# Optimization experiments

Measured on AMD Instinct MI355X. Metric: run time of the kernel, lower is better.

The kernel has to match this reference:

```python
import jax, jax.numpy as jnp
import numpy as np

N = 50000
IN_C, HID_C, OUT_C = 128, 64, 32
E = 800000
NEG_SLOPE = 0.2


def setup_inputs() -> dict:
    key = jax.random.key(0)
    ks = jax.random.split(key, 8)
    x = jax.random.normal(ks[0], (N, IN_C), dtype=jnp.float32)
    edge_index = jax.random.randint(ks[1], (2, E), 0, N, dtype=jnp.int64)
    # GATConv params (heads=1): lin weight, att_src/att_dst vectors, bias
    sc = 1.0 / np.sqrt(IN_C)
    W = jax.random.uniform(ks[2], (IN_C, HID_C), jnp.float32, -sc, sc)
    att_src = jax.random.normal(ks[3], (HID_C,), jnp.float32) * (1.0 / np.sqrt(HID_C))
    att_dst = jax.random.normal(ks[4], (HID_C,), jnp.float32) * (1.0 / np.sqrt(HID_C))
    bias_conv = jnp.zeros((HID_C,), jnp.float32)
    sl = 1.0 / np.sqrt(HID_C)
    W_lin = jax.random.uniform(ks[5], (HID_C, OUT_C), jnp.float32, -sl, sl)
    b_lin = jax.random.uniform(ks[6], (OUT_C,), jnp.float32, -sl, sl)
    return {"x": x, "edge_index": edge_index, "W": W, "att_src": att_src,
            "att_dst": att_dst, "bias_conv": bias_conv, "W_lin": W_lin, "b_lin": b_lin}


def reference(x, edge_index, W, att_src, att_dst, bias_conv, W_lin, b_lin):
    n = x.shape[0]
    h = x @ W  # [N, HID]
    # add self-loops (PyG GATConv default add_self_loops=True)
    loop = jnp.arange(n, dtype=edge_index.dtype)
    src = jnp.concatenate([edge_index[0], loop])  # [E+N]
    dst = jnp.concatenate([edge_index[1], loop])
    a_src = h @ att_src  # [N]
    a_dst = h @ att_dst
    e = jax.nn.leaky_relu(a_src[src] + a_dst[dst], NEG_SLOPE)  # [E+N]
    # segment softmax over incoming edges per destination node
    m = jax.ops.segment_max(e, dst, num_segments=n)
    e = jnp.exp(e - m[dst])
    denom = jax.ops.segment_sum(e, dst, num_segments=n)
    alpha = e / (denom[dst] + 1e-16)
    msg = alpha[:, None] * h[src]  # [E+N, HID]
    out = jax.ops.segment_sum(msg, dst, num_segments=n) + bias_conv
    out = jax.nn.relu(out)
    return out @ W_lin + b_lin
```

## Files before the change

### kernel.cpp

```cpp
#include <hip/hip_runtime.h>
#include <hip/hip_bf16.h>

#define IN_C  128
#define HID_C 64
#define OUT_C 32
#define NEG_SLOPE 0.2f
#define EPB1    2048
#define EPB2    2048
#define BUCKETW 64
#define RCAP    1536
#define SUPW    1024
#define RCAP1   18432
#define PARTS   9
#define CSTRIDE 16
#define XS_LD   136

typedef short bf16x8 __attribute__((ext_vector_type(8)));
typedef float f32x4  __attribute__((ext_vector_type(4)));

__device__ __forceinline__ unsigned short f2bf(float f) {
    __hip_bfloat16 h = __float2bfloat16(f);
    return *(unsigned short*)&h;
}
__device__ __forceinline__ float bflo(unsigned int u) {
    return __uint_as_float(u << 16);
}
__device__ __forceinline__ float bfhi(unsigned int u) {
    return __uint_as_float(u & 0xffff0000u);
}

__global__ __launch_bounds__(256) void gemm_mfma_kernel(
    const float* __restrict__ x, const float* __restrict__ W,
    const float* __restrict__ att_src, const float* __restrict__ att_dst,
    __hip_bfloat16* __restrict__ hb,
    float* __restrict__ a_src, float* __restrict__ a_dst,
    int* __restrict__ bcursor, int ncur, int n_nodes)
{
    __shared__ unsigned short xs[16 * XS_LD];
    __shared__ float redA[4][16];
    __shared__ float redD[4][16];
    const int t    = threadIdx.x;
    const int wv   = t >> 6;
    const int lane = t & 63;
    const int m16  = lane & 15;
    const int quad = lane >> 4;
    const int node0 = blockIdx.x * 16;
    const int nrows = min(16, n_nodes - node0);

    const int gid = blockIdx.x * 256 + t;
    if (gid < ncur) bcursor[gid] = 0;

    const int ncol = wv * 16 + m16;
    bf16x8 B[4];
#pragma unroll
    for (int k0 = 0; k0 < 4; ++k0)
#pragma unroll
        for (int j = 0; j < 8; ++j)
            B[k0][j] = (short)f2bf(W[(k0 * 32 + quad * 8 + j) * HID_C + ncol]);

    {
        const float4* xg = (const float4*)(x + (long)node0 * IN_C);
#pragma unroll
        for (int i = t; i < 512; i += 256) {
            const int row = i >> 5;
            const int c4  = i & 31;
            float4 v = (row < nrows) ? xg[i] : make_float4(0.f, 0.f, 0.f, 0.f);
            ushort4 u;
            u.x = f2bf(v.x); u.y = f2bf(v.y);
            u.z = f2bf(v.z); u.w = f2bf(v.w);
            *(ushort4*)(xs + row * XS_LD + c4 * 4) = u;
        }
    }
    __syncthreads();

    f32x4 C = {0.f, 0.f, 0.f, 0.f};
#pragma unroll
    for (int k0 = 0; k0 < 4; ++k0) {
        const bf16x8 A = *(const bf16x8*)(xs + m16 * XS_LD + k0 * 32 + quad * 8);
        C = __builtin_amdgcn_mfma_f32_16x16x32_bf16(A, B[k0], C, 0, 0, 0);
    }

#pragma unroll
    for (int r = 0; r < 4; ++r) {
        const int row = quad * 4 + r;
        if (row < nrows)
            hb[(long)(node0 + row) * HID_C + ncol] = __float2bfloat16(C[r]);
    }

    {
        const float av = att_src[ncol];
        const float dv = att_dst[ncol];
        float ps[4], pd[4];
#pragma unroll
        for (int r = 0; r < 4; ++r) { ps[r] = C[r] * av; pd[r] = C[r] * dv; }
#pragma unroll
        for (int off = 1; off <= 8; off <<= 1) {
#pragma unroll
            for (int r = 0; r < 4; ++r) {
                ps[r] += __shfl_xor(ps[r], off, 64);
                pd[r] += __shfl_xor(pd[r], off, 64);
            }
        }
        if (m16 == 0) {
#pragma unroll
            for (int r = 0; r < 4; ++r) {
                redA[wv][quad * 4 + r] = ps[r];
                redD[wv][quad * 4 + r] = pd[r];
            }
        }
    }
    __syncthreads();
    if (t < 16 && t < nrows) {
        a_src[node0 + t] = redA[0][t] + redA[1][t] + redA[2][t] + redA[3][t];
        a_dst[node0 + t] = redD[0][t] + redD[1][t] + redD[2][t] + redD[3][t];
    }
}

__global__ __launch_bounds__(256) void bin1_kernel(
    const int* __restrict__ ei, int E,
    int* __restrict__ bcur1, unsigned* __restrict__ superbuf)
{
    __shared__ unsigned stage[EPB1];
    __shared__ int excl[64];
    __shared__ int cur[64];
    __shared__ int gpos[64];

    const int t = threadIdx.x;
    const int base = blockIdx.x * EPB1;
    const int nedge = min(EPB1, E - base);

    if (t < 64) excl[t] = 0;
    __syncthreads();

    for (int i = t; i < nedge; i += 256)
        atomicAdd(&excl[ei[E + base + i] >> 10], 1);
    __syncthreads();

    if (t < 64) {
        int c = excl[t], incl = c;
#pragma unroll
        for (int off = 1; off <= 32; off <<= 1) {
            int u = __shfl_up(incl, off, 64);
            if (t >= off) incl += u;
        }
        excl[t] = incl - c;
        cur[t]  = incl - c;
    }
    __syncthreads();

    for (int i = t; i < nedge; i += 256) {
        const int s = ei[base + i];
        const int d = ei[E + base + i];
        const int sq = d >> 10;
        const int pos = atomicAdd(&cur[sq], 1);
        stage[pos] = (unsigned)s | ((unsigned)(d & 1023) << 16)
                     | ((unsigned)sq << 26);
    }
    __syncthreads();

    if (t < 64) {
        const int c = cur[t] - excl[t];
        gpos[t] = (c > 0) ? atomicAdd(&bcur1[t * CSTRIDE], c) : 0;
    }
    __syncthreads();

    for (int i = t; i < nedge; i += 256) {
        const unsigned r = stage[i];
        const int sq = r >> 26;
        const int dp = gpos[sq] + (i - excl[sq]);
        if (dp < RCAP1) superbuf[(long)sq * RCAP1 + dp] = r;
    }
}

__global__ __launch_bounds__(256) void bin2_kernel(
    const unsigned* __restrict__ superbuf, const int* __restrict__ bcur1,
    int* __restrict__ bcur2, unsigned* __restrict__ bucketbuf)
{
    __shared__ unsigned srt[EPB2];
    __shared__ int cnt[16];
    __shared__ int rp[16];
    __shared__ int cur16[16];
    __shared__ int gpos[16];

    const int t    = threadIdx.x;
    const int sq   = blockIdx.x / PARTS;
    const int part = blockIdx.x % PARTS;
    const int tot  = min(bcur1[sq * CSTRIDE], RCAP1);
    const int beg  = part * EPB2;
    const int n    = min(EPB2, tot - beg);
    if (n <= 0) return;

    if (t < 16) cnt[t] = 0;
    __syncthreads();

    const unsigned* src = superbuf + (long)sq * RCAP1 + beg;

    for (int i = t; i < n; i += 256)
        atomicAdd(&cnt[(src[i] >> 22) & 15], 1);
    __syncthreads();

    if (t == 0) {
        int run = 0;
#pragma unroll
        for (int k = 0; k < 16; ++k) { rp[k] = run; cur16[k] = run; run += cnt[k]; }
    }
    __syncthreads();

    for (int i = t; i < n; i += 256) {
        const unsigned r = src[i];
        const int pos = atomicAdd(&cur16[(r >> 22) & 15], 1);
        srt[pos] = r;
    }
    __syncthreads();

    if (t < 16) {
        const int c = cnt[t];
        const int q2 = sq * 16 + t;
        gpos[t] = (c > 0) ? atomicAdd(&bcur2[q2 * CSTRIDE], c) : 0;
    }
    __syncthreads();

    for (int i = t; i < n; i += 256) {
        const unsigned r = srt[i];
        const int idx = (r >> 22) & 15;
        const int dp  = gpos[idx] + (i - rp[idx]);
        const int q2  = sq * 16 + idx;
        const unsigned nx = (r & 0xFFFFu) | (((r >> 16) & 63u) << 16);
        if (dp < RCAP) bucketbuf[(long)q2 * RCAP + dp] = nx;
    }
}

__global__ __launch_bounds__(512) void bucket_agg_kernel(
    const unsigned* __restrict__ bucketbuf, const int* __restrict__ bcursor,
    const __hip_bfloat16* __restrict__ hb,
    const float* __restrict__ a_src, const float* __restrict__ a_dst,
    const float* __restrict__ bias_conv,
    const float* __restrict__ W_lin, const float* __restrict__ b_lin,
    float* __restrict__ out, int n_nodes)
{
    __shared__ unsigned srtL[RCAP];
    __shared__ int cntd[BUCKETW];
    __shared__ int rp[BUCKETW + 1];
    __shared__ int curd[BUCKETW];

    const int t  = threadIdx.x;
    const int q  = blockIdx.x;
    const int d0 = q * BUCKETW;
    const int dmax = min(BUCKETW, n_nodes - d0);
    const int tot  = min(bcursor[q * CSTRIDE], RCAP);
    const int wv = t >> 6, lane = t & 63, g8 = lane >> 3, l = lane & 7;

    if (t < BUCKETW) cntd[t] = 0;
    __syncthreads();

    const unsigned* gsrc = bucketbuf + (long)q * RCAP;

    for (int i = t; i < tot; i += 512)
        atomicAdd(&cntd[(gsrc[i] >> 16) & 63], 1);
    __syncthreads();

    if (t < 64) {
        int c = cntd[t], incl = c;
#pragma unroll
        for (int off = 1; off <= 32; off <<= 1) {
            int u = __shfl_up(incl, off, 64);
            if (t >= off) incl += u;
        }
        rp[t] = incl - c;
        curd[t] = incl - c;
        if (t == 63) rp[64] = incl;
    }
    __syncthreads();

    for (int i = t; i < tot; i += 512) {
        const unsigned r = gsrc[i];
        const int pos = atomicAdd(&curd[(r >> 16) & 63], 1);
        srtL[pos] = r;
    }
    __syncthreads();

    float Wr[8][4];
#pragma unroll
    for (int kc = 0; kc < 8; ++kc)
#pragma unroll
        for (int kj = 0; kj < 4; ++kj)
            Wr[kc][kj] = W_lin[(l * 8 + kc) * OUT_C + g8 * 4 + kj];
    float biasR[8];
#pragma unroll
    for (int kc = 0; kc < 8; ++kc) biasR[kc] = bias_conv[l * 8 + kc];
    float blinR[4];
#pragma unroll
    for (int kj = 0; kj < 4; ++kj) blinR[kj] = b_lin[g8 * 4 + kj];

    const unsigned short* hbs = (const unsigned short*)hb;

    for (int dloc = wv; dloc < dmax; dloc += 8) {
        const int d = d0 + dloc;
        const float ad = a_dst[d];
        float A[8] = {0.f,0.f,0.f,0.f,0.f,0.f,0.f,0.f};
        float den = 0.f;
        if (g8 == 0) {
            float e = a_src[d] + ad;
            e = (e >= 0.f) ? e : NEG_SLOPE * e;
            const float ws = __expf(e);
            const uint4 hv = *(const uint4*)(hbs + (long)d * HID_C + l * 8);
            den = ws;
            A[0] = ws * bflo(hv.x); A[1] = ws * bfhi(hv.x);
            A[2] = ws * bflo(hv.y); A[3] = ws * bfhi(hv.y);
            A[4] = ws * bflo(hv.z); A[5] = ws * bfhi(hv.z);
            A[6] = ws * bflo(hv.w); A[7] = ws * bfhi(hv.w);
        }
        const int beg = rp[dloc], fin = rp[dloc + 1];
        for (int j = beg + g8; j < fin; j += 16) {
            const int  j1   = j + 8;
            const bool has1 = j1 < fin;
            const unsigned r0 = srtL[j];
            const unsigned r1 = srtL[has1 ? j1 : j];
            const int   s0 = r0 & 0xFFFF;
            const int   s1 = r1 & 0xFFFF;
            const float as0 = a_src[s0];
            const float as1 = a_src[s1];
            const uint4 h0 = *(const uint4*)(hbs + (long)s0 * HID_C + l * 8);
            const uint4 h1 = *(const uint4*)(hbs + (long)s1 * HID_C + l * 8);
            float e0 = as0 + ad; e0 = (e0 >= 0.f) ? e0 : NEG_SLOPE * e0;
            float e1 = as1 + ad; e1 = (e1 >= 0.f) ? e1 : NEG_SLOPE * e1;
            const float w0 = __expf(e0);
            const float w1 = has1 ? __expf(e1) : 0.f;
            den += w0 + w1;
            A[0] = fmaf(w0, bflo(h0.x), A[0]); A[1] = fmaf(w0, bfhi(h0.x), A[1]);
            A[2] = fmaf(w0, bflo(h0.y), A[2]); A[3] = fmaf(w0, bfhi(h0.y), A[3]);
            A[4] = fmaf(w0, bflo(h0.z), A[4]); A[5] = fmaf(w0, bfhi(h0.z), A[5]);
            A[6] = fmaf(w0, bflo(h0.w), A[6]); A[7] = fmaf(w0, bfhi(h0.w), A[7]);
            A[0] = fmaf(w1, bflo(h1.x), A[0]); A[1] = fmaf(w1, bfhi(h1.x), A[1]);
            A[2] = fmaf(w1, bflo(h1.y), A[2]); A[3] = fmaf(w1, bfhi(h1.y), A[3]);
            A[4] = fmaf(w1, bflo(h1.z), A[4]); A[5] = fmaf(w1, bfhi(h1.z), A[5]);
            A[6] = fmaf(w1, bflo(h1.w), A[6]); A[7] = fmaf(w1, bfhi(h1.w), A[7]);
        }
#pragma unroll
        for (int off = 8; off <= 32; off <<= 1) {
#pragma unroll
            for (int k = 0; k < 8; ++k) A[k] += __shfl_xor(A[k], off, 64);
            den += __shfl_xor(den, off, 64);
        }
        const float rd = 1.0f / (den + 1e-16f);
        float p0 = 0.f, p1 = 0.f, p2 = 0.f, p3 = 0.f;
#pragma unroll
        for (int kc = 0; kc < 8; ++kc) {
            float vv = fmaf(A[kc], rd, biasR[kc]);
            vv = vv > 0.f ? vv : 0.f;
            p0 = fmaf(vv, Wr[kc][0], p0);
            p1 = fmaf(vv, Wr[kc][1], p1);
            p2 = fmaf(vv, Wr[kc][2], p2);
            p3 = fmaf(vv, Wr[kc][3], p3);
        }
#pragma unroll
        for (int off = 1; off <= 4; off <<= 1) {
            p0 += __shfl_xor(p0, off, 64);
            p1 += __shfl_xor(p1, off, 64);
            p2 += __shfl_xor(p2, off, 64);
            p3 += __shfl_xor(p3, off, 64);
        }
        if (l == 0) {
            float4 o = make_float4(p0 + blinR[0], p1 + blinR[1],
                                   p2 + blinR[2], p3 + blinR[3]);
            *(float4*)(out + (long)d * OUT_C + g8 * 4) = o;
        }
    }
}

extern "C" void kernel_launch(void* const* d_in, const int* in_sizes, int n_in,
                              void* d_out, int out_size, void* d_ws, size_t ws_size,
                              hipStream_t stream) {
    const float* x         = (const float*)d_in[0];
    const int*   ei        = (const int*)d_in[1];
    const float* W         = (const float*)d_in[2];
    const float* att_src   = (const float*)d_in[3];
    const float* att_dst   = (const float*)d_in[4];
    const float* bias_conv = (const float*)d_in[5];
    const float* W_lin     = (const float*)d_in[6];
    const float* b_lin     = (const float*)d_in[7];
    float*       out       = (float*)d_out;

    const int n_nodes = in_sizes[0] / IN_C;
    const int E       = in_sizes[1] / 2;
    const int B1   = (E + EPB1 - 1) / EPB1;
    const int Q    = (n_nodes + BUCKETW - 1) / BUCKETW;
    const int NSUP = (n_nodes + SUPW - 1) / SUPW;

    __hip_bfloat16* hb = (__hip_bfloat16*)d_ws;
    float* a_src   = (float*)(hb + (long)n_nodes * HID_C);
    float* a_dst   = a_src + n_nodes;
    int*   bcur1   = (int*)(a_dst + n_nodes);
    int*   bcur2   = bcur1 + NSUP * CSTRIDE;
    unsigned* superbuf  = (unsigned*)(bcur2 + (long)Q * CSTRIDE);
    unsigned* bucketbuf = superbuf + (long)NSUP * RCAP1;

    const int ncur = (NSUP + Q) * CSTRIDE;

    gemm_mfma_kernel<<<(n_nodes + 15) / 16, 256, 0, stream>>>(
        x, W, att_src, att_dst, hb, a_src, a_dst,
        bcur1, ncur, n_nodes);

    bin1_kernel<<<B1, 256, 0, stream>>>(ei, E, bcur1, superbuf);

    bin2_kernel<<<NSUP * PARTS, 256, 0, stream>>>(
        superbuf, bcur1, bcur2, bucketbuf);

    bucket_agg_kernel<<<Q, 512, 0, stream>>>(
        bucketbuf, bcur2, hb, a_src, a_dst,
        bias_conv, W_lin, b_lin, out, n_nodes);
}
```

Baseline: 158.6 us.

## Merge GEMM with first binning pass and drop second binning kernel

The node projection GEMM and the first edge-binning pass now run as one launch, with blocks split by index between the two roles, and the cursor zeroing moves to a memset. The second binning kernel is removed; each aggregation block instead scans its whole 1024-node super-bucket and filters the edges that belong to its 64-node bucket. This cuts one launch and one full write and read of the edge list, but each aggregation block now reads about 16 times more edge records, about 16K instead of about 1K.

Measured after the change: 177.8 us. 1.12x slower.

```diff
diff --git a/kernel.cpp b/kernel.cpp
--- a/kernel.cpp
+++ b/kernel.cpp
@@ -6,12 +6,10 @@
 #define OUT_C 32
 #define NEG_SLOPE 0.2f
 #define EPB1    2048
-#define EPB2    2048
 #define BUCKETW 64
 #define RCAP    1536
 #define SUPW    1024
 #define RCAP1   18432
-#define PARTS   9
 #define CSTRIDE 16
 #define XS_LD   136
 
@@ -29,209 +27,148 @@
     return __uint_as_float(u & 0xffff0000u);
 }
 
-__global__ __launch_bounds__(256) void gemm_mfma_kernel(
+__global__ __launch_bounds__(256) void gemm_bin1_kernel(
     const float* __restrict__ x, const float* __restrict__ W,
     const float* __restrict__ att_src, const float* __restrict__ att_dst,
     __hip_bfloat16* __restrict__ hb,
     float* __restrict__ a_src, float* __restrict__ a_dst,
-    int* __restrict__ bcursor, int ncur, int n_nodes)
+    const int* __restrict__ ei, int E,
+    int* __restrict__ bcur1, unsigned* __restrict__ superbuf,
+    int ngemm, int n_nodes)
 {
-    __shared__ unsigned short xs[16 * XS_LD];
-    __shared__ float redA[4][16];
-    __shared__ float redD[4][16];
-    const int t    = threadIdx.x;
-    const int wv   = t >> 6;
-    const int lane = t & 63;
-    const int m16  = lane & 15;
-    const int quad = lane >> 4;
-    const int node0 = blockIdx.x * 16;
-    const int nrows = min(16, n_nodes - node0);
-
-    const int gid = blockIdx.x * 256 + t;
-    if (gid < ncur) bcursor[gid] = 0;
-
-    const int ncol = wv * 16 + m16;
-    bf16x8 B[4];
-#pragma unroll
-    for (int k0 = 0; k0 < 4; ++k0)
-#pragma unroll
-        for (int j = 0; j < 8; ++j)
-            B[k0][j] = (short)f2bf(W[(k0 * 32 + quad * 8 + j) * HID_C + ncol]);
-
-    {
-        const float4* xg = (const float4*)(x + (long)node0 * IN_C);
-#pragma unroll
-        for (int i = t; i < 512; i += 256) {
-            const int row = i >> 5;
-            const int c4  = i & 31;
-            float4 v = (row < nrows) ? xg[i] : make_float4(0.f, 0.f, 0.f, 0.f);
-            ushort4 u;
-            u.x = f2bf(v.x); u.y = f2bf(v.y);
-            u.z = f2bf(v.z); u.w = f2bf(v.w);
-            *(ushort4*)(xs + row * XS_LD + c4 * 4) = u;
-        }
-    }
-    __syncthreads();
-
-    f32x4 C = {0.f, 0.f, 0.f, 0.f};
-#pragma unroll
-    for (int k0 = 0; k0 < 4; ++k0) {
-        const bf16x8 A = *(const bf16x8*)(xs + m16 * XS_LD + k0 * 32 + quad * 8);
-        C = __builtin_amdgcn_mfma_f32_16x16x32_bf16(A, B[k0], C, 0, 0, 0);
-    }
-
-#pragma unroll
-    for (int r = 0; r < 4; ++r) {
-        const int row = quad * 4 + r;
-        if (row < nrows)
-            hb[(long)(node0 + row) * HID_C + ncol] = __float2bfloat16(C[r]);
-    }
-
-    {
-        const float av = att_src[ncol];
-        const float dv = att_dst[ncol];
-        float ps[4], pd[4];
-#pragma unroll
-        for (int r = 0; r < 4; ++r) { ps[r] = C[r] * av; pd[r] = C[r] * dv; }
-#pragma unroll
-        for (int off = 1; off <= 8; off <<= 1) {
-#pragma unroll
-            for (int r = 0; r < 4; ++r) {
-                ps[r] += __shfl_xor(ps[r], off, 64);
-                pd[r] += __shfl_xor(pd[r], off, 64);
+    __shared__ __align__(16) unsigned char smem[8960];
+    const int t = threadIdx.x;
+
+    if ((int)blockIdx.x < ngemm) {
+        unsigned short* xs = (unsigned short*)smem;
+        float (*redA)[16] = (float(*)[16])(smem + 4352);
+        float (*redD)[16] = (float(*)[16])(smem + 4608);
+        const int wv   = t >> 6;
+        const int lane = t & 63;
+        const int m16  = lane & 15;
+        const int quad = lane >> 4;
+        const int node0 = blockIdx.x * 16;
+        const int nrows = min(16, n_nodes - node0);
+
+        const int ncol = wv * 16 + m16;
+        bf16x8 B[4];
+#pragma unroll
+        for (int k0 = 0; k0 < 4; ++k0)
+#pragma unroll
+            for (int j = 0; j < 8; ++j)
+                B[k0][j] = (short)f2bf(W[(k0 * 32 + quad * 8 + j) * HID_C + ncol]);
+
+        {
+            const float4* xg = (const float4*)(x + (long)node0 * IN_C);
+#pragma unroll
+            for (int i = t; i < 512; i += 256) {
+                const int row = i >> 5;
+                const int c4  = i & 31;
+                float4 v = (row < nrows) ? xg[i] : make_float4(0.f, 0.f, 0.f, 0.f);
+                ushort4 u;
+                u.x = f2bf(v.x); u.y = f2bf(v.y);
+                u.z = f2bf(v.z); u.w = f2bf(v.w);
+                *(ushort4*)(xs + row * XS_LD + c4 * 4) = u;
             }
         }
-        if (m16 == 0) {
-#pragma unroll
-            for (int r = 0; r < 4; ++r) {
-                redA[wv][quad * 4 + r] = ps[r];
-                redD[wv][quad * 4 + r] = pd[r];
+        __syncthreads();
+
+        f32x4 C = {0.f, 0.f, 0.f, 0.f};
+#pragma unroll
+        for (int k0 = 0; k0 < 4; ++k0) {
+            const bf16x8 A = *(const bf16x8*)(xs + m16 * XS_LD + k0 * 32 + quad * 8);
+            C = __builtin_amdgcn_mfma_f32_16x16x32_bf16(A, B[k0], C, 0, 0, 0);
+        }
+
+#pragma unroll
+        for (int r = 0; r < 4; ++r) {
+            const int row = quad * 4 + r;
+            if (row < nrows)
+                hb[(long)(node0 + row) * HID_C + ncol] = __float2bfloat16(C[r]);
+        }
+
+        {
+            const float av = att_src[ncol];
+            const float dv = att_dst[ncol];
+            float ps[4], pd[4];
+#pragma unroll
+            for (int r = 0; r < 4; ++r) { ps[r] = C[r] * av; pd[r] = C[r] * dv; }
+#pragma unroll
+            for (int off = 1; off <= 8; off <<= 1) {
+#pragma unroll
+                for (int r = 0; r < 4; ++r) {
+                    ps[r] += __shfl_xor(ps[r], off, 64);
+                    pd[r] += __shfl_xor(pd[r], off, 64);
+                }
             }
-        }
-    }
-    __syncthreads();
-    if (t < 16 && t < nrows) {
-        a_src[node0 + t] = redA[0][t] + redA[1][t] + redA[2][t] + redA[3][t];
-        a_dst[node0 + t] = redD[0][t] + redD[1][t] + redD[2][t] + redD[3][t];
-    }
-}
-
-__global__ __launch_bounds__(256) void bin1_kernel(
-    const int* __restrict__ ei, int E,
-    int* __restrict__ bcur1, unsigned* __restrict__ superbuf)
-{
-    __shared__ unsigned stage[EPB1];
-    __shared__ int excl[64];
-    __shared__ int cur[64];
-    __shared__ int gpos[64];
-
-    const int t = threadIdx.x;
-    const int base = blockIdx.x * EPB1;
-    const int nedge = min(EPB1, E - base);
-
-    if (t < 64) excl[t] = 0;
-    __syncthreads();
-
-    for (int i = t; i < nedge; i += 256)
-        atomicAdd(&excl[ei[E + base + i] >> 10], 1);
-    __syncthreads();
-
-    if (t < 64) {
-        int c = excl[t], incl = c;
-#pragma unroll
-        for (int off = 1; off <= 32; off <<= 1) {
-            int u = __shfl_up(incl, off, 64);
-            if (t >= off) incl += u;
-        }
-        excl[t] = incl - c;
-        cur[t]  = incl - c;
-    }
-    __syncthreads();
-
-    for (int i = t; i < nedge; i += 256) {
-        const int s = ei[base + i];
-        const int d = ei[E + base + i];
-        const int sq = d >> 10;
-        const int pos = atomicAdd(&cur[sq], 1);
-        stage[pos] = (unsigned)s | ((unsigned)(d & 1023) << 16)
-                     | ((unsigned)sq << 26);
-    }
-    __syncthreads();
-
-    if (t < 64) {
-        const int c = cur[t] - excl[t];
-        gpos[t] = (c > 0) ? atomicAdd(&bcur1[t * CSTRIDE], c) : 0;
-    }
-    __syncthreads();
-
-    for (int i = t; i < nedge; i += 256) {
-        const unsigned r = stage[i];
-        const int sq = r >> 26;
-        const int dp = gpos[sq] + (i - excl[sq]);
-        if (dp < RCAP1) superbuf[(long)sq * RCAP1 + dp] = r;
-    }
-}
-
-__global__ __launch_bounds__(256) void bin2_kernel(
+            if (m16 == 0) {
+#pragma unroll
+                for (int r = 0; r < 4; ++r) {
+                    redA[wv][quad * 4 + r] = ps[r];
+                    redD[wv][quad * 4 + r] = pd[r];
+                }
+            }
+        }
+        __syncthreads();
+        if (t < 16 && t < nrows) {
+            a_src[node0 + t] = redA[0][t] + redA[1][t] + redA[2][t] + redA[3][t];
+            a_dst[node0 + t] = redD[0][t] + redD[1][t] + redD[2][t] + redD[3][t];
+        }
+    } else {
+        unsigned* stage = (unsigned*)smem;
+        int* excl = (int*)(smem + 8192);
+        int* cur  = (int*)(smem + 8448);
+        int* gpos = (int*)(smem + 8704);
+
+        const int base = (blockIdx.x - ngemm) * EPB1;
+        const int nedge = min(EPB1, E - base);
+
+        if (t < 64) excl[t] = 0;
+        __syncthreads();
+
+        for (int i = t; i < nedge; i += 256)
+            atomicAdd(&excl[ei[E + base + i] >> 10], 1);
+        __syncthreads();
+
+        if (t < 64) {
+            int c = excl[t], incl = c;
+#pragma unroll
+            for (int off = 1; off <= 32; off <<= 1) {
+                int u = __shfl_up(incl, off, 64);
+                if (t >= off) incl += u;
+            }
+            excl[t] = incl - c;
+            cur[t]  = incl - c;
+        }
+        __syncthreads();
+
+        for (int i = t; i < nedge; i += 256) {
+            const int s = ei[base + i];
+            const int d = ei[E + base + i];
+            const int sq = d >> 10;
+            const int pos = atomicAdd(&cur[sq], 1);
+            stage[pos] = (unsigned)s | ((unsigned)(d & 1023) << 16)
+                         | ((unsigned)sq << 26);
+        }
+        __syncthreads();
+
+        if (t < 64) {
+            const int c = cur[t] - excl[t];
+            gpos[t] = (c > 0) ? atomicAdd(&bcur1[t * CSTRIDE], c) : 0;
+        }
+        __syncthreads();
+
+        for (int i = t; i < nedge; i += 256) {
+            const unsigned r = stage[i];
+            const int sq = r >> 26;
+            const int dp = gpos[sq] + (i - excl[sq]);
+            if (dp < RCAP1) superbuf[(long)sq * RCAP1 + dp] = r;
+        }
+    }
+}
+
+__global__ __launch_bounds__(512) void bucket_agg_kernel(
     const unsigned* __restrict__ superbuf, const int* __restrict__ bcur1,
-    int* __restrict__ bcur2, unsigned* __restrict__ bucketbuf)
-{
-    __shared__ unsigned srt[EPB2];
-    __shared__ int cnt[16];
-    __shared__ int rp[16];
-    __shared__ int cur16[16];
-    __shared__ int gpos[16];
-
-    const int t    = threadIdx.x;
-    const int sq   = blockIdx.x / PARTS;
-    const int part = blockIdx.x % PARTS;
-    const int tot  = min(bcur1[sq * CSTRIDE], RCAP1);
-    const int beg  = part * EPB2;
-    const int n    = min(EPB2, tot - beg);
-    if (n <= 0) return;
-
-    if (t < 16) cnt[t] = 0;
-    __syncthreads();
-
-    const unsigned* src = superbuf + (long)sq * RCAP1 + beg;
-
-    for (int i = t; i < n; i += 256)
-        atomicAdd(&cnt[(src[i] >> 22) & 15], 1);
-    __syncthreads();
-
-    if (t == 0) {
-        int run = 0;
-#pragma unroll
-        for (int k = 0; k < 16; ++k) { rp[k] = run; cur16[k] = run; run += cnt[k]; }
-    }
-    __syncthreads();
-
-    for (int i = t; i < n; i += 256) {
-        const unsigned r = src[i];
-        const int pos = atomicAdd(&cur16[(r >> 22) & 15], 1);
-        srt[pos] = r;
-    }
-    __syncthreads();
-
-    if (t < 16) {
-        const int c = cnt[t];
-        const int q2 = sq * 16 + t;
-        gpos[t] = (c > 0) ? atomicAdd(&bcur2[q2 * CSTRIDE], c) : 0;
-    }
-    __syncthreads();
-
-    for (int i = t; i < n; i += 256) {
-        const unsigned r = srt[i];
-        const int idx = (r >> 22) & 15;
-        const int dp  = gpos[idx] + (i - rp[idx]);
-        const int q2  = sq * 16 + idx;
-        const unsigned nx = (r & 0xFFFFu) | (((r >> 16) & 63u) << 16);
-        if (dp < RCAP) bucketbuf[(long)q2 * RCAP + dp] = nx;
-    }
-}
-
-__global__ __launch_bounds__(512) void bucket_agg_kernel(
-    const unsigned* __restrict__ bucketbuf, const int* __restrict__ bcursor,
     const __hip_bfloat16* __restrict__ hb,
     const float* __restrict__ a_src, const float* __restrict__ a_dst,
     const float* __restrict__ bias_conv,
@@ -243,20 +180,25 @@
     __shared__ int rp[BUCKETW + 1];
     __shared__ int curd[BUCKETW];
 
-    const int t  = threadIdx.x;
-    const int q  = blockIdx.x;
-    const int d0 = q * BUCKETW;
+    const int t   = threadIdx.x;
+    const int q   = blockIdx.x;
+    const int sq  = q >> 4;
+    const int idx = q & 15;
+    const int d0  = q * BUCKETW;
     const int dmax = min(BUCKETW, n_nodes - d0);
-    const int tot  = min(bcursor[q * CSTRIDE], RCAP);
+    const int tot  = min(bcur1[sq * CSTRIDE], RCAP1);
     const int wv = t >> 6, lane = t & 63, g8 = lane >> 3, l = lane & 7;
 
     if (t < BUCKETW) cntd[t] = 0;
     __syncthreads();
 
-    const unsigned* gsrc = bucketbuf + (long)q * RCAP;
-
-    for (int i = t; i < tot; i += 512)
-        atomicAdd(&cntd[(gsrc[i] >> 16) & 63], 1);
+    const unsigned* src = superbuf + (long)sq * RCAP1;
+
+    for (int i = t; i < tot; i += 512) {
+        const unsigned r = src[i];
+        if (((r >> 22) & 15) == (unsigned)idx)
+            atomicAdd(&cntd[(r >> 16) & 63], 1);
+    }
     __syncthreads();
 
     if (t < 64) {
@@ -273,9 +215,11 @@
     __syncthreads();
 
     for (int i = t; i < tot; i += 512) {
-        const unsigned r = gsrc[i];
-        const int pos = atomicAdd(&curd[(r >> 16) & 63], 1);
-        srtL[pos] = r;
+        const unsigned r = src[i];
+        if (((r >> 22) & 15) == (unsigned)idx) {
+            const int pos = atomicAdd(&curd[(r >> 16) & 63], 1);
+            if (pos < RCAP) srtL[pos] = r;
+        }
     }
     __syncthreads();
 
@@ -310,7 +254,8 @@
             A[4] = ws * bflo(hv.z); A[5] = ws * bfhi(hv.z);
             A[6] = ws * bflo(hv.w); A[7] = ws * bfhi(hv.w);
         }
-        const int beg = rp[dloc], fin = rp[dloc + 1];
+        const int beg = min(rp[dloc], RCAP);
+        const int fin = min(rp[dloc + 1], RCAP);
         for (int j = beg + g8; j < fin; j += 16) {
             const int  j1   = j + 8;
             const bool has1 = j1 < fin;
@@ -386,27 +331,21 @@
     const int B1   = (E + EPB1 - 1) / EPB1;
     const int Q    = (n_nodes + BUCKETW - 1) / BUCKETW;
     const int NSUP = (n_nodes + SUPW - 1) / SUPW;
+    const int NG   = (n_nodes + 15) / 16;
 
     __hip_bfloat16* hb = (__hip_bfloat16*)d_ws;
     float* a_src   = (float*)(hb + (long)n_nodes * HID_C);
     float* a_dst   = a_src + n_nodes;
     int*   bcur1   = (int*)(a_dst + n_nodes);
-    int*   bcur2   = bcur1 + NSUP * CSTRIDE;
-    unsigned* superbuf  = (unsigned*)(bcur2 + (long)Q * CSTRIDE);
-    unsigned* bucketbuf = superbuf + (long)NSUP * RCAP1;
-
-    const int ncur = (NSUP + Q) * CSTRIDE;
-
-    gemm_mfma_kernel<<<(n_nodes + 15) / 16, 256, 0, stream>>>(
+    unsigned* superbuf = (unsigned*)(bcur1 + NSUP * CSTRIDE);
+
+    hipMemsetAsync(bcur1, 0, (size_t)NSUP * CSTRIDE * sizeof(int), stream);
+
+    gemm_bin1_kernel<<<NG + B1, 256, 0, stream>>>(
         x, W, att_src, att_dst, hb, a_src, a_dst,
-        bcur1, ncur, n_nodes);
-
-    bin1_kernel<<<B1, 256, 0, stream>>>(ei, E, bcur1, superbuf);
-
-    bin2_kernel<<<NSUP * PARTS, 256, 0, stream>>>(
-        superbuf, bcur1, bcur2, bucketbuf);
+        ei, E, bcur1, superbuf, NG, n_nodes);
 
     bucket_agg_kernel<<<Q, 512, 0, stream>>>(
-        bucketbuf, bcur2, hb, a_src, a_dst,
+        superbuf, bcur1, hb, a_src, a_dst,
         bias_conv, W_lin, b_lin, out, n_nodes);
 }
```

## Fuse GEMM and first edge-binning pass into one heterogeneous kernel launch

Applied to the files above, without the earlier changes.

Merges the node-feature GEMM kernel and the first binning kernel into a single launch, with block ranges selecting which role each block plays and a shared byte buffer reinterpreted per role. The two stages are independent, so binning can overlap with the GEMM instead of waiting behind it, and one launch gap is removed. Cursor zeroing moves out of the GEMM into a separate memset, which adds a small extra operation on the stream.

New measurement: 156.0 us, median of 2. No clear change (-1.7%).

```diff
diff --git a/kernel.cpp b/kernel.cpp
--- a/kernel.cpp
+++ b/kernel.cpp
@@ -29,146 +29,143 @@
     return __uint_as_float(u & 0xffff0000u);
 }
 
-__global__ __launch_bounds__(256) void gemm_mfma_kernel(
+__global__ __launch_bounds__(256) void gemm_bin1_kernel(
     const float* __restrict__ x, const float* __restrict__ W,
     const float* __restrict__ att_src, const float* __restrict__ att_dst,
     __hip_bfloat16* __restrict__ hb,
     float* __restrict__ a_src, float* __restrict__ a_dst,
-    int* __restrict__ bcursor, int ncur, int n_nodes)
+    const int* __restrict__ ei, int E,
+    int* __restrict__ bcur1, unsigned* __restrict__ superbuf,
+    int ngemm, int n_nodes)
 {
-    __shared__ unsigned short xs[16 * XS_LD];
-    __shared__ float redA[4][16];
-    __shared__ float redD[4][16];
-    const int t    = threadIdx.x;
-    const int wv   = t >> 6;
-    const int lane = t & 63;
-    const int m16  = lane & 15;
-    const int quad = lane >> 4;
-    const int node0 = blockIdx.x * 16;
-    const int nrows = min(16, n_nodes - node0);
-
-    const int gid = blockIdx.x * 256 + t;
-    if (gid < ncur) bcursor[gid] = 0;
-
-    const int ncol = wv * 16 + m16;
-    bf16x8 B[4];
-#pragma unroll
-    for (int k0 = 0; k0 < 4; ++k0)
-#pragma unroll
-        for (int j = 0; j < 8; ++j)
-            B[k0][j] = (short)f2bf(W[(k0 * 32 + quad * 8 + j) * HID_C + ncol]);
-
-    {
-        const float4* xg = (const float4*)(x + (long)node0 * IN_C);
-#pragma unroll
-        for (int i = t; i < 512; i += 256) {
-            const int row = i >> 5;
-            const int c4  = i & 31;
-            float4 v = (row < nrows) ? xg[i] : make_float4(0.f, 0.f, 0.f, 0.f);
-            ushort4 u;
-            u.x = f2bf(v.x); u.y = f2bf(v.y);
-            u.z = f2bf(v.z); u.w = f2bf(v.w);
-            *(ushort4*)(xs + row * XS_LD + c4 * 4) = u;
-        }
-    }
-    __syncthreads();
-
-    f32x4 C = {0.f, 0.f, 0.f, 0.f};
-#pragma unroll
-    for (int k0 = 0; k0 < 4; ++k0) {
-        const bf16x8 A = *(const bf16x8*)(xs + m16 * XS_LD + k0 * 32 + quad * 8);
-        C = __builtin_amdgcn_mfma_f32_16x16x32_bf16(A, B[k0], C, 0, 0, 0);
-    }
-
-#pragma unroll
-    for (int r = 0; r < 4; ++r) {
-        const int row = quad * 4 + r;
-        if (row < nrows)
-            hb[(long)(node0 + row) * HID_C + ncol] = __float2bfloat16(C[r]);
-    }
-
-    {
-        const float av = att_src[ncol];
-        const float dv = att_dst[ncol];
-        float ps[4], pd[4];
-#pragma unroll
-        for (int r = 0; r < 4; ++r) { ps[r] = C[r] * av; pd[r] = C[r] * dv; }
-#pragma unroll
-        for (int off = 1; off <= 8; off <<= 1) {
-#pragma unroll
-            for (int r = 0; r < 4; ++r) {
-                ps[r] += __shfl_xor(ps[r], off, 64);
-                pd[r] += __shfl_xor(pd[r], off, 64);
+    __shared__ __align__(16) unsigned char smem[8960];
+    const int t = threadIdx.x;
+
+    if ((int)blockIdx.x < ngemm) {
+        unsigned short* xs = (unsigned short*)smem;
+        float (*redA)[16] = (float(*)[16])(smem + 4352);
+        float (*redD)[16] = (float(*)[16])(smem + 4608);
+        const int wv   = t >> 6;
+        const int lane = t & 63;
+        const int m16  = lane & 15;
+        const int quad = lane >> 4;
+        const int node0 = blockIdx.x * 16;
+        const int nrows = min(16, n_nodes - node0);
+
+        const int ncol = wv * 16 + m16;
+        bf16x8 B[4];
+#pragma unroll
+        for (int k0 = 0; k0 < 4; ++k0)
+#pragma unroll
+            for (int j = 0; j < 8; ++j)
+                B[k0][j] = (short)f2bf(W[(k0 * 32 + quad * 8 + j) * HID_C + ncol]);
+
+        {
+            const float4* xg = (const float4*)(x + (long)node0 * IN_C);
+#pragma unroll
+            for (int i = t; i < 512; i += 256) {
+                const int row = i >> 5;
+                const int c4  = i & 31;
+                float4 v = (row < nrows) ? xg[i] : make_float4(0.f, 0.f, 0.f, 0.f);
+                ushort4 u;
+                u.x = f2bf(v.x); u.y = f2bf(v.y);
+                u.z = f2bf(v.z); u.w = f2bf(v.w);
+                *(ushort4*)(xs + row * XS_LD + c4 * 4) = u;
             }
         }
-        if (m16 == 0) {
-#pragma unroll
-            for (int r = 0; r < 4; ++r) {
-                redA[wv][quad * 4 + r] = ps[r];
-                redD[wv][quad * 4 + r] = pd[r];
+        __syncthreads();
+
+        f32x4 C = {0.f, 0.f, 0.f, 0.f};
+#pragma unroll
+        for (int k0 = 0; k0 < 4; ++k0) {
+            const bf16x8 A = *(const bf16x8*)(xs + m16 * XS_LD + k0 * 32 + quad * 8);
+            C = __builtin_amdgcn_mfma_f32_16x16x32_bf16(A, B[k0], C, 0, 0, 0);
+        }
+
+#pragma unroll
+        for (int r = 0; r < 4; ++r) {
+            const int row = quad * 4 + r;
+            if (row < nrows)
+                hb[(long)(node0 + row) * HID_C + ncol] = __float2bfloat16(C[r]);
+        }
+
+        {
+            const float av = att_src[ncol];
+            const float dv = att_dst[ncol];
+            float ps[4], pd[4];
+#pragma unroll
+            for (int r = 0; r < 4; ++r) { ps[r] = C[r] * av; pd[r] = C[r] * dv; }
+#pragma unroll
+            for (int off = 1; off <= 8; off <<= 1) {
+#pragma unroll
+                for (int r = 0; r < 4; ++r) {
+                    ps[r] += __shfl_xor(ps[r], off, 64);
+                    pd[r] += __shfl_xor(pd[r], off, 64);
+                }
             }
-        }
-    }
-    __syncthreads();
-    if (t < 16 && t < nrows) {
-        a_src[node0 + t] = redA[0][t] + redA[1][t] + redA[2][t] + redA[3][t];
-        a_dst[node0 + t] = redD[0][t] + redD[1][t] + redD[2][t] + redD[3][t];
-    }
-}
-
-__global__ __launch_bounds__(256) void bin1_kernel(
-    const int* __restrict__ ei, int E,
-    int* __restrict__ bcur1, unsigned* __restrict__ superbuf)
-{
-    __shared__ unsigned stage[EPB1];
-    __shared__ int excl[64];
-    __shared__ int cur[64];
-    __shared__ int gpos[64];
-
-    const int t = threadIdx.x;
-    const int base = blockIdx.x * EPB1;
-    const int nedge = min(EPB1, E - base);
-
-    if (t < 64) excl[t] = 0;
-    __syncthreads();
-
-    for (int i = t; i < nedge; i += 256)
-        atomicAdd(&excl[ei[E + base + i] >> 10], 1);
-    __syncthreads();
-
-    if (t < 64) {
-        int c = excl[t], incl = c;
-#pragma unroll
-        for (int off = 1; off <= 32; off <<= 1) {
-            int u = __shfl_up(incl, off, 64);
-            if (t >= off) incl += u;
-        }
-        excl[t] = incl - c;
-        cur[t]  = incl - c;
-    }
-    __syncthreads();
-
-    for (int i = t; i < nedge; i += 256) {
-        const int s = ei[base + i];
-        const int d = ei[E + base + i];
-        const int sq = d >> 10;
-        const int pos = atomicAdd(&cur[sq], 1);
-        stage[pos] = (unsigned)s | ((unsigned)(d & 1023) << 16)
-                     | ((unsigned)sq << 26);
-    }
-    __syncthreads();
-
-    if (t < 64) {
-        const int c = cur[t] - excl[t];
-        gpos[t] = (c > 0) ? atomicAdd(&bcur1[t * CSTRIDE], c) : 0;
-    }
-    __syncthreads();
-
-    for (int i = t; i < nedge; i += 256) {
-        const unsigned r = stage[i];
-        const int sq = r >> 26;
-        const int dp = gpos[sq] + (i - excl[sq]);
-        if (dp < RCAP1) superbuf[(long)sq * RCAP1 + dp] = r;
+            if (m16 == 0) {
+#pragma unroll
+                for (int r = 0; r < 4; ++r) {
+                    redA[wv][quad * 4 + r] = ps[r];
+                    redD[wv][quad * 4 + r] = pd[r];
+                }
+            }
+        }
+        __syncthreads();
+        if (t < 16 && t < nrows) {
+            a_src[node0 + t] = redA[0][t] + redA[1][t] + redA[2][t] + redA[3][t];
+            a_dst[node0 + t] = redD[0][t] + redD[1][t] + redD[2][t] + redD[3][t];
+        }
+    } else {
+        unsigned* stage = (unsigned*)smem;
+        int* excl = (int*)(smem + 8192);
+        int* cur  = (int*)(smem + 8448);
+        int* gpos = (int*)(smem + 8704);
+
+        const int base = (blockIdx.x - ngemm) * EPB1;
+        const int nedge = min(EPB1, E - base);
+
+        if (t < 64) excl[t] = 0;
+        __syncthreads();
+
+        for (int i = t; i < nedge; i += 256)
+            atomicAdd(&excl[ei[E + base + i] >> 10], 1);
+        __syncthreads();
+
+        if (t < 64) {
+            int c = excl[t], incl = c;
+#pragma unroll
+            for (int off = 1; off <= 32; off <<= 1) {
+                int u = __shfl_up(incl, off, 64);
+                if (t >= off) incl += u;
+            }
+            excl[t] = incl - c;
+            cur[t]  = incl - c;
+        }
+        __syncthreads();
+
+        for (int i = t; i < nedge; i += 256) {
+            const int s = ei[base + i];
+            const int d = ei[E + base + i];
+            const int sq = d >> 10;
+            const int pos = atomicAdd(&cur[sq], 1);
+            stage[pos] = (unsigned)s | ((unsigned)(d & 1023) << 16)
+                         | ((unsigned)sq << 26);
+        }
+        __syncthreads();
+
+        if (t < 64) {
+            const int c = cur[t] - excl[t];
+            gpos[t] = (c > 0) ? atomicAdd(&bcur1[t * CSTRIDE], c) : 0;
+        }
+        __syncthreads();
+
+        for (int i = t; i < nedge; i += 256) {
+            const unsigned r = stage[i];
+            const int sq = r >> 26;
+            const int dp = gpos[sq] + (i - excl[sq]);
+            if (dp < RCAP1) superbuf[(long)sq * RCAP1 + dp] = r;
+        }
     }
 }
 
@@ -386,6 +383,7 @@
     const int B1   = (E + EPB1 - 1) / EPB1;
     const int Q    = (n_nodes + BUCKETW - 1) / BUCKETW;
     const int NSUP = (n_nodes + SUPW - 1) / SUPW;
+    const int NG   = (n_nodes + 15) / 16;
 
     __hip_bfloat16* hb = (__hip_bfloat16*)d_ws;
     float* a_src   = (float*)(hb + (long)n_nodes * HID_C);
@@ -395,13 +393,12 @@
     unsigned* superbuf  = (unsigned*)(bcur2 + (long)Q * CSTRIDE);
     unsigned* bucketbuf = superbuf + (long)NSUP * RCAP1;
 
-    const int ncur = (NSUP + Q) * CSTRIDE;
-
-    gemm_mfma_kernel<<<(n_nodes + 15) / 16, 256, 0, stream>>>(
+    hipMemsetAsync(bcur1, 0,
+                   (size_t)(NSUP + Q) * CSTRIDE * sizeof(int), stream);
+
+    gemm_bin1_kernel<<<NG + B1, 256, 0, stream>>>(
         x, W, att_src, att_dst, hb, a_src, a_dst,
-        bcur1, ncur, n_nodes);
-
-    bin1_kernel<<<B1, 256, 0, stream>>>(ei, E, bcur1, superbuf);
+        ei, E, bcur1, superbuf, NG, n_nodes);
 
     bin2_kernel<<<NSUP * PARTS, 256, 0, stream>>>(
         superbuf, bcur1, bcur2, bucketbuf);
```
